# Kernel optimization log

Measured on AMD Instinct MI355X. Metric: run time of the kernel, lower is better.

## Reference

```python
import jax, jax.numpy as jnp
import numpy as np
from jax import lax

BN_EPS = 1e-5
PAD = ((2, 3), (1, 2))  # 'same' padding for kernel (6,4): H pad 5 -> (2,3), W pad 3 -> (1,2)
DN = ('NCHW', 'OIHW', 'NCHW')


def _conv_block(x, w, b, g, bt, m, v, pool):
    # pool(bn(relu(conv(pad(x))))) as in the torch module (eval-mode BN)
    x = lax.conv_general_dilated(x, w, (1, 1), PAD, dimension_numbers=DN)
    x = jax.nn.relu(x + b[None, :, None, None])
    scale = g / jnp.sqrt(v + BN_EPS)
    x = (x - m[None, :, None, None]) * scale[None, :, None, None] + bt[None, :, None, None]
    win = (1, 1) + pool
    return lax.reduce_window(x, -jnp.inf, lax.max, win, win, 'VALID')


def _fc_bn(x, w, b, g, bt, m, v):
    x = jax.nn.relu(x @ w.T + b)
    return (x - m) * (g / jnp.sqrt(v + BN_EPS)) + bt


def _apply_cnn(x, p):
    x = x[:, None, :, :]  # [N,1,72,64]
    x = _conv_block(x, p['conv1_w'], p['conv1_b'], p['bnc1_g'], p['bnc1_b'], p['bnc1_m'], p['bnc1_v'], (2, 2))
    x = _conv_block(x, p['conv2_w'], p['conv2_b'], p['bnc2_g'], p['bnc2_b'], p['bnc2_m'], p['bnc2_v'], (2, 2))
    x = _conv_block(x, p['conv3_w'], p['conv3_b'], p['bnc3_g'], p['bnc3_b'], p['bnc3_m'], p['bnc3_v'], (3, 4))
    x = x.reshape(x.shape[0], 6 * 4 * 64)  # NCHW contiguous flatten matches torch .view
    x = _fc_bn(x, p['fc1_w'], p['fc1_b'], p['bnf1_g'], p['bnf1_b'], p['bnf1_m'], p['bnf1_v'])
    x = _fc_bn(x, p['fc2_w'], p['fc2_b'], p['bnf2_g'], p['bnf2_b'], p['bnf2_m'], p['bnf2_v'])
    x = _fc_bn(x, p['fc3_w'], p['fc3_b'], p['bnf3_g'], p['bnf3_b'], p['bnf3_m'], p['bnf3_v'])
    # F.normalize(x, p=2, dim=1) with eps=1e-12
    nrm = jnp.linalg.norm(x, axis=1, keepdims=True)
    return x / jnp.maximum(nrm, 1e-12)


def _ssm(embeds):
    # pairwise L2 distances via Gram trick (replaces the O(n^2) python loop)
    sq = jnp.sum(embeds * embeds, axis=1)  # [n]
    d2 = sq[:, None] + sq[None, :] - 2.0 * (embeds @ embeds.T)
    dist = jnp.sqrt(jnp.maximum(d2, 1e-12))
    dist = jnp.where(d2 > 0, dist, 0.0)  # exact zeros on diagonal, nan-safe grad
    return dist / jnp.max(dist)


def setup_inputs() -> dict:
    key = jax.random.key(0)
    ks = iter(jax.random.split(key, 64))
    d = {'x': jax.random.normal(next(ks), (512, 72, 64), jnp.float32)}

    def nrm(shape, s=0.05):
        return jax.random.normal(next(ks), shape, jnp.float32) * s

    def add_bn(name, c):
        d[name + '_g'] = 1.0 + nrm((c,))
        d[name + '_b'] = nrm((c,))
        d[name + '_m'] = nrm((c,), 0.1)
        d[name + '_v'] = 0.5 + jax.random.uniform(next(ks), (c,), jnp.float32)

    d['conv1_w'] = nrm((16, 1, 6, 4), 0.2);  d['conv1_b'] = nrm((16,));  add_bn('bnc1', 16)
    d['conv2_w'] = nrm((32, 16, 6, 4), 0.1); d['conv2_b'] = nrm((32,));  add_bn('bnc2', 32)
    d['conv3_w'] = nrm((64, 32, 6, 4), 0.05); d['conv3_b'] = nrm((64,)); add_bn('bnc3', 64)
    d['fc1_w'] = nrm((512, 1536), 0.03); d['fc1_b'] = nrm((512,)); add_bn('bnf1', 512)
    d['fc2_w'] = nrm((256, 512), 0.05);  d['fc2_b'] = nrm((256,)); add_bn('bnf2', 256)
    d['fc3_w'] = nrm((128, 256), 0.07);  d['fc3_b'] = nrm((128,)); add_bn('bnf3', 128)
    return d


def reference(x,
              conv1_w, conv1_b, bnc1_g, bnc1_b, bnc1_m, bnc1_v,
              conv2_w, conv2_b, bnc2_g, bnc2_b, bnc2_m, bnc2_v,
              conv3_w, conv3_b, bnc3_g, bnc3_b, bnc3_m, bnc3_v,
              fc1_w, fc1_b, bnf1_g, bnf1_b, bnf1_m, bnf1_v,
              fc2_w, fc2_b, bnf2_g, bnf2_b, bnf2_m, bnf2_v,
              fc3_w, fc3_b, bnf3_g, bnf3_b, bnf3_m, bnf3_v):
    p = dict(conv1_w=conv1_w, conv1_b=conv1_b, bnc1_g=bnc1_g, bnc1_b=bnc1_b, bnc1_m=bnc1_m, bnc1_v=bnc1_v,
             conv2_w=conv2_w, conv2_b=conv2_b, bnc2_g=bnc2_g, bnc2_b=bnc2_b, bnc2_m=bnc2_m, bnc2_v=bnc2_v,
             conv3_w=conv3_w, conv3_b=conv3_b, bnc3_g=bnc3_g, bnc3_b=bnc3_b, bnc3_m=bnc3_m, bnc3_v=bnc3_v,
             fc1_w=fc1_w, fc1_b=fc1_b, bnf1_g=bnf1_g, bnf1_b=bnf1_b, bnf1_m=bnf1_m, bnf1_v=bnf1_v,
             fc2_w=fc2_w, fc2_b=fc2_b, bnf2_g=bnf2_g, bnf2_b=bnf2_b, bnf2_m=bnf2_m, bnf2_v=bnf2_v,
             fc3_w=fc3_w, fc3_b=fc3_b, bnf3_g=bnf3_g, bnf3_b=bnf3_b, bnf3_m=bnf3_m, bnf3_v=bnf3_v)
    embeds = _apply_cnn(x, p)  # [n, 128], L2-normalized
    return _ssm(embeds)        # [n, n]
```

## Files before the change

### kernel.cpp

```cpp
#include <hip/hip_runtime.h>
#include <hip/hip_bf16.h>
#include <math.h>


#define BN_EPS 1e-5f

typedef __attribute__((ext_vector_type(8))) short short8;
typedef __attribute__((ext_vector_type(4))) float f32x4;

__device__ __forceinline__ unsigned short f2bf(float f) {
    unsigned u = __float_as_uint(f);
    u += 0x7fffu + ((u >> 16) & 1u);
    return (unsigned short)(u >> 16);
}

__device__ __forceinline__ unsigned pkbf(float a, float b) {
    __hip_bfloat162 h = __float22bfloat162_rn(make_float2(a, b));
    return *reinterpret_cast<unsigned*>(&h);
}

__global__ __launch_bounds__(256) void repack_k(
    const float* __restrict__ w1, const float* __restrict__ w2,
    const float* __restrict__ w3,
    const float* __restrict__ fw1, const float* __restrict__ fw2,
    const float* __restrict__ fw3,
    unsigned short* __restrict__ wT1b,
    unsigned short* __restrict__ wT2b, unsigned short* __restrict__ wT3b,
    unsigned short* __restrict__ fw1b, unsigned short* __restrict__ fw2b,
    unsigned short* __restrict__ fw3b)
{
    int t = blockIdx.x * 256 + threadIdx.x;
    if (t < 512) {
        int k = t & 31, oc = t >> 5;
        wT1b[t] = (k < 24) ? f2bf(w1[oc * 24 + k]) : (unsigned short)0;
    }
    if (t < 12288) {
        int k = t & 31, oc = (t >> 5) & 31, kk = t >> 10;
        int ky = kk >> 1, kxp = kk & 1;
        int hi = k >> 4, ic = k & 15;
        int kx = 2 * kxp + hi;
        wT2b[t] = f2bf(w2[((oc * 16 + ic) * 6 + ky) * 4 + kx]);
    }
    if (t < 49152) {
        int ic = t & 31, oc = (t >> 5) & 63, kk = t >> 11;
        int ky = kk >> 2, kx = kk & 3;
        wT3b[t] = f2bf(w3[((oc * 32 + ic) * 6 + ky) * 4 + kx]);
    }
    if (t < 786432) fw1b[t] = f2bf(fw1[t]);
    if (t < 131072) fw2b[t] = f2bf(fw2[t]);
    if (t < 32768)  fw3b[t] = f2bf(fw3[t]);
}

__global__ __launch_bounds__(256) void conv1_mf(
    const float* __restrict__ x, const unsigned short* __restrict__ wT1,
    const float* __restrict__ bias, const float* __restrict__ g,
    const float* __restrict__ bt, const float* __restrict__ m,
    const float* __restrict__ v, unsigned short* __restrict__ out1,
    int nb0)
{
    __shared__ __align__(16) float pa[79 * 68];
    __shared__ __align__(16) float pb[79 * 68];
    const int tid = threadIdx.x, nl = blockIdx.x;
    {
        float2 z2 = make_float2(0.f, 0.f);
        float2* za = (float2*)pa; float2* zb = (float2*)pb;
        for (int i = tid; i < 2686; i += 256) { za[i] = z2; zb[i] = z2; }
    }
    unsigned short* ob = out1 + (size_t)nl * 23616;
    {
        uint4 z; z.x = z.y = z.z = z.w = 0u;
        for (int pc = tid; pc < 324; pc += 256) {
            int row, colc;
            if (pc < 180) { row = pc / 36; colc = pc % 36; if (row >= 2) row += 36; }
            else { int pz = pc - 180; row = 2 + (pz >> 2); colc = (pz & 3) ? 32 + (pz & 3) : 0; }
            uint4* d = (uint4*)(ob + ((size_t)row * 36 + colc) * 16);
            d[0] = z; d[1] = z;
        }
    }
    __syncthreads();
    {
        const float4* src = (const float4*)(x + (size_t)(nb0 + nl) * 4608);
        for (int i = tid; i < 1152; i += 256) {
            float4 val = src[i];
            int f = i * 4;
            int row = (f >> 6) + 2, c = (f & 63) + 1;
            float* a = pa + row * 68 + c;
            a[0] = val.x; a[1] = val.y; a[2] = val.z; a[3] = val.w;
            float2* b = (float2*)(pb + row * 68 + c + 1);
            b[0] = make_float2(val.x, val.y);
            b[1] = make_float2(val.z, val.w);
        }
    }
    const int lane = tid & 63, wave = tid >> 6;
    const int n = lane & 15, q = lane >> 4;
    float sc = g[n] * rsqrtf(v[n] + BN_EPS);
    float bb = bias[n];
    float mm = bt[n] - m[n] * sc;
    short8 bfr = *(const short8*)(wT1 + n * 32 + q * 8);
    __syncthreads();

    for (int i = 0; i < 72; ++i) {
        int t = wave * 72 + i;
        int pooled = 4 * t + (n >> 2);
        int ph = pooled >> 5, pw = pooled & 31;
        int py = (n >> 1) & 1, px = n & 1;
        int oh = 2 * ph + py, ow = 2 * pw + px;
        int r0 = (oh + 2 * q) * 68;
        const float* base = px ? (pb + r0 + ow + 1) : (pa + r0 + ow);
        float2 s00 = *(const float2*)(base);
        float2 s01 = *(const float2*)(base + 2);
        float2 s10 = *(const float2*)(base + 68);
        float2 s11 = *(const float2*)(base + 70);
        uint4 uu;
        uu.x = pkbf(s00.x, s00.y); uu.y = pkbf(s01.x, s01.y);
        uu.z = pkbf(s10.x, s10.y); uu.w = pkbf(s11.x, s11.y);
        short8 afr = *reinterpret_cast<short8*>(&uu);
        f32x4 acc = (f32x4){0.f, 0.f, 0.f, 0.f};
        acc = __builtin_amdgcn_mfma_f32_16x16x32_bf16(afr, bfr, acc, 0, 0, 0);
        int po = 4 * t + q;
        int oph = po >> 5, opw = po & 31;
        float mx = fmaxf(fmaxf(acc[0], acc[1]), fmaxf(acc[2], acc[3]));
        float val = fmaxf(mx + bb, 0.f) * sc + mm;
        ob[((size_t)(oph + 2) * 36 + (opw + 1)) * 16 + n] = f2bf(val);
    }
}

__global__ __launch_bounds__(256) void conv2_m(
    const unsigned short* __restrict__ in, const unsigned short* __restrict__ wT,
    const float* __restrict__ bias, const float* __restrict__ g,
    const float* __restrict__ bt, const float* __restrict__ m,
    const float* __restrict__ v, unsigned short* __restrict__ out)
{
    __shared__ __align__(16) unsigned short in_s[41 * 36 * 16];
    const int tid = threadIdx.x, nl = blockIdx.x;
    {
        const uint4* src = (const uint4*)(in + (size_t)nl * 23616);
        uint4* dst = (uint4*)in_s;
        for (int i = tid; i < 2952; i += 256) dst[i] = src[i];
    }
    unsigned short* ob = out + (size_t)nl * 15360;
    {
        uint4 z; z.x = z.y = z.z = z.w = 0u;
        for (int pc = tid; pc < 192; pc += 256) {
            int row, colc;
            if (pc < 120) { row = pc / 20; colc = pc % 20; if (row >= 2) row += 18; }
            else { int pz = pc - 120; row = 2 + (pz >> 2); colc = (pz & 3) ? 16 + (pz & 3) : 0; }
            uint4* d = (uint4*)(ob + ((size_t)row * 20 + colc) * 32);
            d[0] = z; d[1] = z; d[2] = z; d[3] = z;
        }
    }
    const int lane = tid & 63, wave = tid >> 6;
    const int n = lane & 15, q = lane >> 4;
    float bnb[2], bns[2], bnm[2];
#pragma unroll
    for (int nt = 0; nt < 2; ++nt) {
        int oc = nt * 16 + n;
        float sc = g[oc] * rsqrtf(v[oc] + BN_EPS);
        bnb[nt] = bias[oc]; bns[nt] = sc; bnm[nt] = bt[oc] - m[oc] * sc;
    }
    __syncthreads();

    for (int pass = 0; pass < 3; ++pass) {
        f32x4 acc[3][2][2];
#pragma unroll
        for (int j = 0; j < 3; ++j)
#pragma unroll
            for (int ab = 0; ab < 2; ++ab)
#pragma unroll
                for (int nt = 0; nt < 2; ++nt)
                    acc[j][ab][nt] = (f32x4){0.f, 0.f, 0.f, 0.f};

#pragma unroll
        for (int ky = 0; ky < 6; ++ky)
#pragma unroll
            for (int kxp = 0; kxp < 2; ++kxp) {
                int kk = ky * 2 + kxp;
                short8 bfr[2];
#pragma unroll
                for (int nt = 0; nt < 2; ++nt)
                    bfr[nt] = *(const short8*)(wT + (((size_t)kk * 32 + nt * 16 + n) * 32 + q * 8));
#pragma unroll
                for (int j = 0; j < 3; ++j) {
                    int pp = wave + 4 * (pass * 3 + j);
                    int ph = pp >> 1, half = pp & 1;
                    int col = half * 16 + n + 2 * kxp;
#pragma unroll
                    for (int ab = 0; ab < 2; ++ab) {
                        int row = 2 * ph + ab + ky;
                        short8 afr = *(const short8*)(in_s + (((size_t)row * 36 + col) * 16 + q * 8));
                        acc[j][ab][0] = __builtin_amdgcn_mfma_f32_16x16x32_bf16(afr, bfr[0], acc[j][ab][0], 0, 0, 0);
                        acc[j][ab][1] = __builtin_amdgcn_mfma_f32_16x16x32_bf16(afr, bfr[1], acc[j][ab][1], 0, 0, 0);
                    }
                }
            }
#pragma unroll
        for (int j = 0; j < 3; ++j) {
            int pp = wave + 4 * (pass * 3 + j);
            int ph = pp >> 1, half = pp & 1;
            int pw0 = half * 8 + q * 2;
#pragma unroll
            for (int nt = 0; nt < 2; ++nt) {
                int oc = nt * 16 + n;
                float p0 = fmaxf(fmaxf(acc[j][0][nt][0], acc[j][0][nt][1]),
                                 fmaxf(acc[j][1][nt][0], acc[j][1][nt][1]));
                float p1 = fmaxf(fmaxf(acc[j][0][nt][2], acc[j][0][nt][3]),
                                 fmaxf(acc[j][1][nt][2], acc[j][1][nt][3]));
                p0 = fmaxf(p0 + bnb[nt], 0.f) * bns[nt] + bnm[nt];
                p1 = fmaxf(p1 + bnb[nt], 0.f) * bns[nt] + bnm[nt];
                ob[((size_t)(ph + 2) * 20 + (pw0 + 1)) * 32 + oc] = f2bf(p0);
                ob[((size_t)(ph + 2) * 20 + (pw0 + 2)) * 32 + oc] = f2bf(p1);
            }
        }
    }
}

__global__ __launch_bounds__(384) void conv3_m(
    const unsigned short* __restrict__ in, const unsigned short* __restrict__ wT,
    const float* __restrict__ bias, const float* __restrict__ g,
    const float* __restrict__ bt, const float* __restrict__ m,
    const float* __restrict__ v, unsigned short* __restrict__ out3, int nb0)
{
    __shared__ __align__(16) unsigned short in_s[24 * 20 * 32];
    const int tid = threadIdx.x, nl = blockIdx.x;
    {
        const uint4* src = (const uint4*)(in + (size_t)nl * 15360);
        uint4* dst = (uint4*)in_s;
        for (int i = tid; i < 1920; i += 384) dst[i] = src[i];
    }
    const int lane = tid & 63, pr = tid >> 6;
    const int n = lane & 15, q = lane >> 4;
    float bnb[4], bns[4], bnm[4];
#pragma unroll
    for (int nt = 0; nt < 4; ++nt) {
        int oc = nt * 16 + n;
        float sc = g[oc] * rsqrtf(v[oc] + BN_EPS);
        bnb[nt] = bias[oc]; bns[nt] = sc; bnm[nt] = bt[oc] - m[oc] * sc;
    }
    __syncthreads();

    f32x4 acc[3][4];
#pragma unroll
    for (int r = 0; r < 3; ++r)
#pragma unroll
        for (int nt = 0; nt < 4; ++nt) acc[r][nt] = (f32x4){0.f, 0.f, 0.f, 0.f};

#pragma unroll
    for (int ky = 0; ky < 6; ++ky)
#pragma unroll
        for (int kx = 0; kx < 4; ++kx) {
            int kk = ky * 4 + kx;
            short8 bfr[4];
#pragma unroll
            for (int nt = 0; nt < 4; ++nt)
                bfr[nt] = *(const short8*)(wT + (((size_t)kk * 64 + nt * 16 + n) * 32 + q * 8));
#pragma unroll
            for (int r = 0; r < 3; ++r) {
                int row = 3 * pr + r + ky;
                int col = n + kx;
                short8 afr = *(const short8*)(in_s + (((size_t)row * 20 + col) * 32 + q * 8));
#pragma unroll
                for (int nt = 0; nt < 4; ++nt)
                    acc[r][nt] = __builtin_amdgcn_mfma_f32_16x16x32_bf16(afr, bfr[nt], acc[r][nt], 0, 0, 0);
            }
        }
    size_t ob = (size_t)(nb0 + nl) * 1536;
#pragma unroll
    for (int nt = 0; nt < 4; ++nt) {
        float mx = -3.4e38f;
#pragma unroll
        for (int r = 0; r < 3; ++r)
#pragma unroll
            for (int e = 0; e < 4; ++e) mx = fmaxf(mx, acc[r][nt][e]);
        float val = fmaxf(mx + bnb[nt], 0.f) * bns[nt] + bnm[nt];
        out3[ob + (size_t)(nt * 16 + n) * 24 + pr * 4 + q] = f2bf(val);
    }
}

__global__ __launch_bounds__(256) void fc_m(
    const unsigned short* __restrict__ A, const unsigned short* __restrict__ W,
    const float* __restrict__ bias, const float* __restrict__ g,
    const float* __restrict__ bt, const float* __restrict__ m,
    const float* __restrict__ v, unsigned short* __restrict__ out_b,
    float* __restrict__ out_f, int K, int N, int mode)
{
    const int tid = threadIdx.x;
    const int lane = tid & 63, wave = tid >> 6;
    const int n = lane & 15, q = lane >> 4;
    const int wr = wave >> 1, wc = wave & 1;
    const int r0 = blockIdx.y * 32 + wr * 16;
    const int c0 = blockIdx.x * 32 + wc * 16;
    const int col = c0 + n;

    float sc = g[col] * rsqrtf(v[col] + BN_EPS);
    float bb = bias[col];
    float mm = bt[col] - m[col] * sc;

    const unsigned short* Ap = A + (size_t)(r0 + n) * K + q * 8;
    const unsigned short* Bp = W + (size_t)col * K + q * 8;

    f32x4 acc = (f32x4){0.f, 0.f, 0.f, 0.f};
    for (int kk = 0; kk < K; kk += 64) {
        short8 a0 = *(const short8*)(Ap + kk);
        short8 b0 = *(const short8*)(Bp + kk);
        short8 a1 = *(const short8*)(Ap + kk + 32);
        short8 b1 = *(const short8*)(Bp + kk + 32);
        acc = __builtin_amdgcn_mfma_f32_16x16x32_bf16(a0, b0, acc, 0, 0, 0);
        acc = __builtin_amdgcn_mfma_f32_16x16x32_bf16(a1, b1, acc, 0, 0, 0);
    }
#pragma unroll
    for (int e = 0; e < 4; ++e) {
        int row = r0 + q * 4 + e;
        float val = fmaxf(acc[e] + bb, 0.f) * sc + mm;
        if (mode == 0) out_b[(size_t)row * N + col] = f2bf(val);
        else           out_f[(size_t)row * N + col] = val;
    }
}

__global__ __launch_bounds__(128) void norm_k(const float* __restrict__ f3,
                                              float* __restrict__ E,
                                              float* __restrict__ sq)
{
    __shared__ float red[2];
    const int row = blockIdx.x, tid = threadIdx.x;
    float vv = f3[row * 128 + tid];
    float s = vv * vv;
#pragma unroll
    for (int off = 32; off >= 1; off >>= 1) s += __shfl_down(s, off, 64);
    if ((tid & 63) == 0) red[tid >> 6] = s;
    __syncthreads();
    float total = red[0] + red[1];
    float nn = fmaxf(sqrtf(total), 1e-12f);
    E[row * 128 + tid] = vv / nn;
    if (tid == 0) sq[row] = total / (nn * nn);
}

__global__ __launch_bounds__(256) void dist_k(const float* __restrict__ E,
                                              const float* __restrict__ sq,
                                              float* __restrict__ D,
                                              unsigned* __restrict__ mxslot)
{
    __shared__ __align__(16) float Ei[16 * 132];
    __shared__ __align__(16) float Ej[16 * 132];
    __shared__ float red[256];
    const int tid = threadIdx.x;
    const int bi = blockIdx.y * 16, bj = blockIdx.x * 16;
    {
        int lr = tid >> 4, lc = (tid & 15) * 8;
        float4 a0 = *(const float4*)(E + (bi + lr) * 128 + lc);
        float4 a1 = *(const float4*)(E + (bi + lr) * 128 + lc + 4);
        *(float4*)(Ei + lr * 132 + lc) = a0;
        *(float4*)(Ei + lr * 132 + lc + 4) = a1;
        float4 b0 = *(const float4*)(E + (bj + lr) * 128 + lc);
        float4 b1 = *(const float4*)(E + (bj + lr) * 128 + lc + 4);
        *(float4*)(Ej + lr * 132 + lc) = b0;
        *(float4*)(Ej + lr * 132 + lc + 4) = b1;
    }
    __syncthreads();
    const int tx = tid & 15, ty = tid >> 4;
    float dot = 0.f;
#pragma unroll 4
    for (int k = 0; k < 128; k += 4) {
        float4 a = *(const float4*)(Ei + ty * 132 + k);
        float4 b = *(const float4*)(Ej + tx * 132 + k);
        dot = fmaf(a.x, b.x, dot); dot = fmaf(a.y, b.y, dot);
        dot = fmaf(a.z, b.z, dot); dot = fmaf(a.w, b.w, dot);
    }
    int i = bi + ty, j = bj + tx;
    float d2 = sq[i] + sq[j] - 2.f * dot;
    float dist = sqrtf(fmaxf(d2, 1e-12f));
    dist = (d2 > 0.f) ? dist : 0.f;
    if (i == j) dist = 0.f;
    D[i * 512 + j] = dist;
    red[tid] = dist;
    __syncthreads();
    for (int s2 = 128; s2 > 0; s2 >>= 1) {
        if (tid < s2) red[tid] = fmaxf(red[tid], red[tid + s2]);
        __syncthreads();
    }
    if (tid == 0) atomicMax(mxslot, __float_as_uint(red[0]));
}

__global__ __launch_bounds__(256) void scale_k(float* __restrict__ D,
                                               const unsigned* __restrict__ mxslot)
{
    int idx = blockIdx.x * 256 + threadIdx.x;
    float M = __uint_as_float(*mxslot);
    D[idx] = D[idx] / M;
}

extern "C" void kernel_launch(void* const* d_in, const int* in_sizes, int n_in,
                              void* d_out, int out_size, void* d_ws, size_t ws_size,
                              hipStream_t stream)
{
    (void)in_sizes; (void)n_in; (void)out_size;
    const float* x    = (const float*)d_in[0];
    const float* c1w  = (const float*)d_in[1];
    const float* c1b  = (const float*)d_in[2];
    const float* g1   = (const float*)d_in[3];
    const float* b1   = (const float*)d_in[4];
    const float* m1   = (const float*)d_in[5];
    const float* v1   = (const float*)d_in[6];
    const float* c2w  = (const float*)d_in[7];
    const float* c2b  = (const float*)d_in[8];
    const float* g2   = (const float*)d_in[9];
    const float* b2   = (const float*)d_in[10];
    const float* m2   = (const float*)d_in[11];
    const float* v2   = (const float*)d_in[12];
    const float* c3w  = (const float*)d_in[13];
    const float* c3b  = (const float*)d_in[14];
    const float* g3   = (const float*)d_in[15];
    const float* b3   = (const float*)d_in[16];
    const float* m3   = (const float*)d_in[17];
    const float* v3   = (const float*)d_in[18];
    const float* fw1  = (const float*)d_in[19];
    const float* fb1  = (const float*)d_in[20];
    const float* gf1  = (const float*)d_in[21];
    const float* bf1  = (const float*)d_in[22];
    const float* mf1  = (const float*)d_in[23];
    const float* vf1  = (const float*)d_in[24];
    const float* fw2  = (const float*)d_in[25];
    const float* fb2  = (const float*)d_in[26];
    const float* gf2  = (const float*)d_in[27];
    const float* bf2  = (const float*)d_in[28];
    const float* mf2  = (const float*)d_in[29];
    const float* vf2  = (const float*)d_in[30];
    const float* fw3  = (const float*)d_in[31];
    const float* fb3  = (const float*)d_in[32];
    const float* gf3  = (const float*)d_in[33];
    const float* bf3  = (const float*)d_in[34];
    const float* mf3  = (const float*)d_in[35];
    const float* vf3  = (const float*)d_in[36];

    float* ws = (float*)d_ws;
    float* f3v  = ws + 0;
    float* E    = ws + 65536;
    float* sq   = ws + 131072;
    unsigned* mx = (unsigned*)(ws + 131584);
    unsigned short* wT2b = (unsigned short*)(ws + 131600);
    unsigned short* wT3b = (unsigned short*)(ws + 137744);
    unsigned short* wT1b = (unsigned short*)(ws + 162320);
    unsigned short* fw1b = (unsigned short*)(ws + 162576);
    unsigned short* fw2b = (unsigned short*)(ws + 555792);
    unsigned short* fw3b = (unsigned short*)(ws + 621328);
    unsigned short* out3b= (unsigned short*)(ws + 637712);
    unsigned short* a1b  = (unsigned short*)(ws + 1030928);
    unsigned short* a2b  = (unsigned short*)(ws + 1162000);
    const size_t CH0 = 1227536;

    int Bc = 512;
    while (Bc > 4 && (size_t)CH0 * 4 + (size_t)Bc * 77952 > ws_size) Bc >>= 1;
    unsigned short* out1c = (unsigned short*)(ws + CH0);
    unsigned short* out2c = out1c + (size_t)Bc * 23616;

    float* out = (float*)d_out;

    hipMemsetAsync(mx, 0, 4, stream);
    repack_k<<<3072, 256, 0, stream>>>(c1w, c2w, c3w, fw1, fw2, fw3,
                                       wT1b, wT2b, wT3b, fw1b, fw2b, fw3b);
    for (int nb0 = 0; nb0 < 512; nb0 += Bc) {
        conv1_mf<<<Bc, 256, 0, stream>>>(x, wT1b, c1b, g1, b1, m1, v1, out1c, nb0);
        conv2_m<<<Bc, 256, 0, stream>>>(out1c, wT2b, c2b, g2, b2, m2, v2, out2c);
        conv3_m<<<Bc, 384, 0, stream>>>(out2c, wT3b, c3b, g3, b3, m3, v3, out3b, nb0);
    }
    fc_m<<<dim3(16, 16), 256, 0, stream>>>(out3b, fw1b, fb1, gf1, bf1, mf1, vf1,
                                           a1b, nullptr, 1536, 512, 0);
    fc_m<<<dim3(8, 16), 256, 0, stream>>>(a1b, fw2b, fb2, gf2, bf2, mf2, vf2,
                                          a2b, nullptr, 512, 256, 0);
    fc_m<<<dim3(4, 16), 256, 0, stream>>>(a2b, fw3b, fb3, gf3, bf3, mf3, vf3,
                                          nullptr, f3v, 256, 128, 1);
    norm_k<<<512, 128, 0, stream>>>(f3v, E, sq);
    dist_k<<<dim3(32, 32), 256, 0, stream>>>(E, sq, out, mx);
    scale_k<<<1024, 256, 0, stream>>>(out, mx);
}
```

Before: 239.5 us.

## Fuse three conv stages into one LDS-resident kernel and fuse FC chain with normalize

Merges conv1, conv2 and conv3 into a single 512-thread kernel per sample that keeps the intermediate activations in shared memory instead of global workspace. Conv1 input is converted to bf16 while staging, which halves LDS use and removes per-MFMA packing. The three FC layers and L2 normalization are fused into one kernel that keeps intermediates in LDS, and the memset is folded into repack. This removes global round-trips and several launches, at the cost of higher per-block LDS use and fewer blocks for the FC stage (32 blocks), which may lower parallelism.

```diff
diff --git a/kernel.cpp b/kernel.cpp
--- a/kernel.cpp
+++ b/kernel.cpp
@@ -1,5 +1,4 @@
 #include <hip/hip_runtime.h>
-#include <hip/hip_bf16.h>
 #include <math.h>
 
 
@@ -12,11 +11,6 @@
     unsigned u = __float_as_uint(f);
     u += 0x7fffu + ((u >> 16) & 1u);
     return (unsigned short)(u >> 16);
-}
-
-__device__ __forceinline__ unsigned pkbf(float a, float b) {
-    __hip_bfloat162 h = __float22bfloat162_rn(make_float2(a, b));
-    return *reinterpret_cast<unsigned*>(&h);
 }
 
 __global__ __launch_bounds__(256) void repack_k(
@@ -27,9 +21,10 @@
     unsigned short* __restrict__ wT1b,
     unsigned short* __restrict__ wT2b, unsigned short* __restrict__ wT3b,
     unsigned short* __restrict__ fw1b, unsigned short* __restrict__ fw2b,
-    unsigned short* __restrict__ fw3b)
+    unsigned short* __restrict__ fw3b, unsigned* __restrict__ mxslot)
 {
     int t = blockIdx.x * 256 + threadIdx.x;
+    if (t == 0) *mxslot = 0u;
     if (t < 512) {
         int k = t & 31, oc = t >> 5;
         wT1b[t] = (k < 24) ? f2bf(w1[oc * 24 + k]) : (unsigned short)0;
@@ -51,287 +46,276 @@
     if (t < 32768)  fw3b[t] = f2bf(fw3[t]);
 }
 
-__global__ __launch_bounds__(256) void conv1_mf(
+__global__ __launch_bounds__(512) void conv_all(
     const float* __restrict__ x, const unsigned short* __restrict__ wT1,
-    const float* __restrict__ bias, const float* __restrict__ g,
-    const float* __restrict__ bt, const float* __restrict__ m,
-    const float* __restrict__ v, unsigned short* __restrict__ out1,
-    int nb0)
-{
-    __shared__ __align__(16) float pa[79 * 68];
-    __shared__ __align__(16) float pb[79 * 68];
+    const unsigned short* __restrict__ wT2, const unsigned short* __restrict__ wT3,
+    const float* __restrict__ c1b, const float* __restrict__ g1,
+    const float* __restrict__ b1, const float* __restrict__ m1,
+    const float* __restrict__ v1,
+    const float* __restrict__ c2b, const float* __restrict__ g2,
+    const float* __restrict__ b2, const float* __restrict__ m2,
+    const float* __restrict__ v2,
+    const float* __restrict__ c3b, const float* __restrict__ g3,
+    const float* __restrict__ b3, const float* __restrict__ m3,
+    const float* __restrict__ v3,
+    unsigned short* __restrict__ out3)
+{
+    __shared__ __align__(16) unsigned short s_out1[41 * 36 * 16];
+    __shared__ __align__(16) unsigned short s_un[24 * 20 * 32];
     const int tid = threadIdx.x, nl = blockIdx.x;
+    const int lane = tid & 63, wave = tid >> 6;
+    const int n = lane & 15, q = lane >> 4;
+    unsigned short* pa = s_un;
+    unsigned short* pb = s_un + 5372;
+
     {
-        float2 z2 = make_float2(0.f, 0.f);
-        float2* za = (float2*)pa; float2* zb = (float2*)pb;
-        for (int i = tid; i < 2686; i += 256) { za[i] = z2; zb[i] = z2; }
-    }
-    unsigned short* ob = out1 + (size_t)nl * 23616;
-    {
-        uint4 z; z.x = z.y = z.z = z.w = 0u;
-        for (int pc = tid; pc < 324; pc += 256) {
+        unsigned* z32 = (unsigned*)s_un;
+        for (int i = tid; i < 5372; i += 512) z32[i] = 0u;
+        uint4 z4; z4.x = z4.y = z4.z = z4.w = 0u;
+        for (int pc = tid; pc < 324; pc += 512) {
             int row, colc;
             if (pc < 180) { row = pc / 36; colc = pc % 36; if (row >= 2) row += 36; }
             else { int pz = pc - 180; row = 2 + (pz >> 2); colc = (pz & 3) ? 32 + (pz & 3) : 0; }
-            uint4* d = (uint4*)(ob + ((size_t)row * 36 + colc) * 16);
-            d[0] = z; d[1] = z;
+            uint4* d = (uint4*)(s_out1 + ((size_t)row * 36 + colc) * 16);
+            d[0] = z4; d[1] = z4;
         }
     }
     __syncthreads();
     {
-        const float4* src = (const float4*)(x + (size_t)(nb0 + nl) * 4608);
-        for (int i = tid; i < 1152; i += 256) {
+        const float4* src = (const float4*)(x + (size_t)nl * 4608);
+        for (int i = tid; i < 1152; i += 512) {
             float4 val = src[i];
-            int f = i * 4;
-            int row = (f >> 6) + 2, c = (f & 63) + 1;
-            float* a = pa + row * 68 + c;
-            a[0] = val.x; a[1] = val.y; a[2] = val.z; a[3] = val.w;
-            float2* b = (float2*)(pb + row * 68 + c + 1);
-            b[0] = make_float2(val.x, val.y);
-            b[1] = make_float2(val.z, val.w);
-        }
-    }
-    const int lane = tid & 63, wave = tid >> 6;
-    const int n = lane & 15, q = lane >> 4;
-    float sc = g[n] * rsqrtf(v[n] + BN_EPS);
-    float bb = bias[n];
-    float mm = bt[n] - m[n] * sc;
-    short8 bfr = *(const short8*)(wT1 + n * 32 + q * 8);
-    __syncthreads();
-
-    for (int i = 0; i < 72; ++i) {
-        int t = wave * 72 + i;
+            int f = i * 4, row = (f >> 6) + 2, c = (f & 63) + 1;
+            unsigned short h0 = f2bf(val.x), h1 = f2bf(val.y);
+            unsigned short h2 = f2bf(val.z), h3 = f2bf(val.w);
+            unsigned short* ap = pa + row * 68 + c;
+            ap[0] = h0; ap[1] = h1; ap[2] = h2; ap[3] = h3;
+            unsigned* bp = (unsigned*)(pb + row * 68 + c + 1);
+            bp[0] = (unsigned)h0 | ((unsigned)h1 << 16);
+            bp[1] = (unsigned)h2 | ((unsigned)h3 << 16);
+        }
+    }
+    const float sc1 = g1[n] * rsqrtf(v1[n] + BN_EPS);
+    const float bb1 = c1b[n];
+    const float mm1 = b1[n] - m1[n] * sc1;
+    const short8 bfr1 = *(const short8*)(wT1 + n * 32 + q * 8);
+    __syncthreads();
+
+    for (int i = 0; i < 36; ++i) {
+        int t = wave * 36 + i;
         int pooled = 4 * t + (n >> 2);
         int ph = pooled >> 5, pw = pooled & 31;
         int py = (n >> 1) & 1, px = n & 1;
         int oh = 2 * ph + py, ow = 2 * pw + px;
         int r0 = (oh + 2 * q) * 68;
-        const float* base = px ? (pb + r0 + ow + 1) : (pa + r0 + ow);
-        float2 s00 = *(const float2*)(base);
-        float2 s01 = *(const float2*)(base + 2);
-        float2 s10 = *(const float2*)(base + 68);
-        float2 s11 = *(const float2*)(base + 70);
+        const unsigned* base = px ? (const unsigned*)(pb + r0 + ow + 1)
+                                  : (const unsigned*)(pa + r0 + ow);
         uint4 uu;
-        uu.x = pkbf(s00.x, s00.y); uu.y = pkbf(s01.x, s01.y);
-        uu.z = pkbf(s10.x, s10.y); uu.w = pkbf(s11.x, s11.y);
+        uu.x = base[0];  uu.y = base[1];
+        uu.z = base[34]; uu.w = base[35];
         short8 afr = *reinterpret_cast<short8*>(&uu);
         f32x4 acc = (f32x4){0.f, 0.f, 0.f, 0.f};
-        acc = __builtin_amdgcn_mfma_f32_16x16x32_bf16(afr, bfr, acc, 0, 0, 0);
-        int po = 4 * t + q;
-        int oph = po >> 5, opw = po & 31;
+        acc = __builtin_amdgcn_mfma_f32_16x16x32_bf16(afr, bfr1, acc, 0, 0, 0);
+        int po = 4 * t + q, oph = po >> 5, opw = po & 31;
         float mx = fmaxf(fmaxf(acc[0], acc[1]), fmaxf(acc[2], acc[3]));
-        float val = fmaxf(mx + bb, 0.f) * sc + mm;
-        ob[((size_t)(oph + 2) * 36 + (opw + 1)) * 16 + n] = f2bf(val);
-    }
-}
-
-__global__ __launch_bounds__(256) void conv2_m(
-    const unsigned short* __restrict__ in, const unsigned short* __restrict__ wT,
-    const float* __restrict__ bias, const float* __restrict__ g,
-    const float* __restrict__ bt, const float* __restrict__ m,
-    const float* __restrict__ v, unsigned short* __restrict__ out)
-{
-    __shared__ __align__(16) unsigned short in_s[41 * 36 * 16];
-    const int tid = threadIdx.x, nl = blockIdx.x;
+        float val = fmaxf(mx + bb1, 0.f) * sc1 + mm1;
+        s_out1[((oph + 2) * 36 + (opw + 1)) * 16 + n] = f2bf(val);
+    }
+    __syncthreads();
     {
-        const uint4* src = (const uint4*)(in + (size_t)nl * 23616);
-        uint4* dst = (uint4*)in_s;
-        for (int i = tid; i < 2952; i += 256) dst[i] = src[i];
-    }
-    unsigned short* ob = out + (size_t)nl * 15360;
-    {
-        uint4 z; z.x = z.y = z.z = z.w = 0u;
-        for (int pc = tid; pc < 192; pc += 256) {
+        uint4 z4; z4.x = z4.y = z4.z = z4.w = 0u;
+        for (int pc = tid; pc < 192; pc += 512) {
             int row, colc;
             if (pc < 120) { row = pc / 20; colc = pc % 20; if (row >= 2) row += 18; }
             else { int pz = pc - 120; row = 2 + (pz >> 2); colc = (pz & 3) ? 16 + (pz & 3) : 0; }
-            uint4* d = (uint4*)(ob + ((size_t)row * 20 + colc) * 32);
-            d[0] = z; d[1] = z; d[2] = z; d[3] = z;
-        }
-    }
-    const int lane = tid & 63, wave = tid >> 6;
-    const int n = lane & 15, q = lane >> 4;
-    float bnb[2], bns[2], bnm[2];
+            uint4* d = (uint4*)(s_un + ((size_t)row * 20 + colc) * 32);
+            d[0] = z4; d[1] = z4; d[2] = z4; d[3] = z4;
+        }
+    }
+    float bnb2[2], bns2[2], bnm2[2];
 #pragma unroll
     for (int nt = 0; nt < 2; ++nt) {
         int oc = nt * 16 + n;
-        float sc = g[oc] * rsqrtf(v[oc] + BN_EPS);
-        bnb[nt] = bias[oc]; bns[nt] = sc; bnm[nt] = bt[oc] - m[oc] * sc;
-    }
-    __syncthreads();
-
-    for (int pass = 0; pass < 3; ++pass) {
-        f32x4 acc[3][2][2];
-#pragma unroll
-        for (int j = 0; j < 3; ++j)
-#pragma unroll
-            for (int ab = 0; ab < 2; ++ab)
-#pragma unroll
-                for (int nt = 0; nt < 2; ++nt)
-                    acc[j][ab][nt] = (f32x4){0.f, 0.f, 0.f, 0.f};
-
+        float sc = g2[oc] * rsqrtf(v2[oc] + BN_EPS);
+        bnb2[nt] = c2b[oc]; bns2[nt] = sc; bnm2[nt] = b2[oc] - m2[oc] * sc;
+    }
+    __syncthreads();
+
+    for (int pp = wave; pp < 36; pp += 8) {
+        int ph = pp >> 1, half = pp & 1;
+        f32x4 acc[2][2];
+#pragma unroll
+        for (int ab = 0; ab < 2; ++ab)
+#pragma unroll
+            for (int nt = 0; nt < 2; ++nt) acc[ab][nt] = (f32x4){0.f, 0.f, 0.f, 0.f};
 #pragma unroll
         for (int ky = 0; ky < 6; ++ky)
 #pragma unroll
             for (int kxp = 0; kxp < 2; ++kxp) {
                 int kk = ky * 2 + kxp;
-                short8 bfr[2];
-#pragma unroll
-                for (int nt = 0; nt < 2; ++nt)
-                    bfr[nt] = *(const short8*)(wT + (((size_t)kk * 32 + nt * 16 + n) * 32 + q * 8));
-#pragma unroll
-                for (int j = 0; j < 3; ++j) {
-                    int pp = wave + 4 * (pass * 3 + j);
-                    int ph = pp >> 1, half = pp & 1;
-                    int col = half * 16 + n + 2 * kxp;
-#pragma unroll
-                    for (int ab = 0; ab < 2; ++ab) {
-                        int row = 2 * ph + ab + ky;
-                        short8 afr = *(const short8*)(in_s + (((size_t)row * 36 + col) * 16 + q * 8));
-                        acc[j][ab][0] = __builtin_amdgcn_mfma_f32_16x16x32_bf16(afr, bfr[0], acc[j][ab][0], 0, 0, 0);
-                        acc[j][ab][1] = __builtin_amdgcn_mfma_f32_16x16x32_bf16(afr, bfr[1], acc[j][ab][1], 0, 0, 0);
-                    }
+                short8 w0 = *(const short8*)(wT2 + ((size_t)(kk * 32 + n) * 32) + q * 8);
+                short8 w1 = *(const short8*)(wT2 + ((size_t)(kk * 32 + 16 + n) * 32) + q * 8);
+                int col = half * 16 + n + 2 * kxp;
+#pragma unroll
+                for (int ab = 0; ab < 2; ++ab) {
+                    int row = 2 * ph + ab + ky;
+                    short8 afr = *(const short8*)(s_out1 + ((size_t)(row * 36 + col) * 16) + q * 8);
+                    acc[ab][0] = __builtin_amdgcn_mfma_f32_16x16x32_bf16(afr, w0, acc[ab][0], 0, 0, 0);
+                    acc[ab][1] = __builtin_amdgcn_mfma_f32_16x16x32_bf16(afr, w1, acc[ab][1], 0, 0, 0);
                 }
             }
-#pragma unroll
-        for (int j = 0; j < 3; ++j) {
-            int pp = wave + 4 * (pass * 3 + j);
-            int ph = pp >> 1, half = pp & 1;
-            int pw0 = half * 8 + q * 2;
-#pragma unroll
-            for (int nt = 0; nt < 2; ++nt) {
-                int oc = nt * 16 + n;
-                float p0 = fmaxf(fmaxf(acc[j][0][nt][0], acc[j][0][nt][1]),
-                                 fmaxf(acc[j][1][nt][0], acc[j][1][nt][1]));
-                float p1 = fmaxf(fmaxf(acc[j][0][nt][2], acc[j][0][nt][3]),
-                                 fmaxf(acc[j][1][nt][2], acc[j][1][nt][3]));
-                p0 = fmaxf(p0 + bnb[nt], 0.f) * bns[nt] + bnm[nt];
-                p1 = fmaxf(p1 + bnb[nt], 0.f) * bns[nt] + bnm[nt];
-                ob[((size_t)(ph + 2) * 20 + (pw0 + 1)) * 32 + oc] = f2bf(p0);
-                ob[((size_t)(ph + 2) * 20 + (pw0 + 2)) * 32 + oc] = f2bf(p1);
+        int pw0 = half * 8 + q * 2;
+#pragma unroll
+        for (int nt = 0; nt < 2; ++nt) {
+            int oc = nt * 16 + n;
+            float p0 = fmaxf(fmaxf(acc[0][nt][0], acc[0][nt][1]),
+                             fmaxf(acc[1][nt][0], acc[1][nt][1]));
+            float p1 = fmaxf(fmaxf(acc[0][nt][2], acc[0][nt][3]),
+                             fmaxf(acc[1][nt][2], acc[1][nt][3]));
+            p0 = fmaxf(p0 + bnb2[nt], 0.f) * bns2[nt] + bnm2[nt];
+            p1 = fmaxf(p1 + bnb2[nt], 0.f) * bns2[nt] + bnm2[nt];
+            s_un[((size_t)(ph + 2) * 20 + (pw0 + 1)) * 32 + oc] = f2bf(p0);
+            s_un[((size_t)(ph + 2) * 20 + (pw0 + 2)) * 32 + oc] = f2bf(p1);
+        }
+    }
+    __syncthreads();
+
+    for (int ch = wave; ch < 12; ch += 8) {
+        int pr = ch >> 1, nth = ch & 1;
+        f32x4 acc[3][2];
+#pragma unroll
+        for (int r = 0; r < 3; ++r)
+#pragma unroll
+            for (int t2 = 0; t2 < 2; ++t2) acc[r][t2] = (f32x4){0.f, 0.f, 0.f, 0.f};
+#pragma unroll
+        for (int ky = 0; ky < 6; ++ky)
+#pragma unroll
+            for (int kx = 0; kx < 4; ++kx) {
+                int kk = ky * 4 + kx;
+                short8 w0 = *(const short8*)(wT3 + ((size_t)(kk * 64 + nth * 32 + n) * 32) + q * 8);
+                short8 w1 = *(const short8*)(wT3 + ((size_t)(kk * 64 + nth * 32 + 16 + n) * 32) + q * 8);
+#pragma unroll
+                for (int r = 0; r < 3; ++r) {
+                    int row = 3 * pr + r + ky;
+                    int col = n + kx;
+                    short8 afr = *(const short8*)(s_un + ((size_t)(row * 20 + col) * 32) + q * 8);
+                    acc[r][0] = __builtin_amdgcn_mfma_f32_16x16x32_bf16(afr, w0, acc[r][0], 0, 0, 0);
+                    acc[r][1] = __builtin_amdgcn_mfma_f32_16x16x32_bf16(afr, w1, acc[r][1], 0, 0, 0);
+                }
             }
-        }
-    }
-}
-
-__global__ __launch_bounds__(384) void conv3_m(
-    const unsigned short* __restrict__ in, const unsigned short* __restrict__ wT,
-    const float* __restrict__ bias, const float* __restrict__ g,
-    const float* __restrict__ bt, const float* __restrict__ m,
-    const float* __restrict__ v, unsigned short* __restrict__ out3, int nb0)
-{
-    __shared__ __align__(16) unsigned short in_s[24 * 20 * 32];
-    const int tid = threadIdx.x, nl = blockIdx.x;
-    {
-        const uint4* src = (const uint4*)(in + (size_t)nl * 15360);
-        uint4* dst = (uint4*)in_s;
-        for (int i = tid; i < 1920; i += 384) dst[i] = src[i];
-    }
-    const int lane = tid & 63, pr = tid >> 6;
-    const int n = lane & 15, q = lane >> 4;
-    float bnb[4], bns[4], bnm[4];
-#pragma unroll
-    for (int nt = 0; nt < 4; ++nt) {
-        int oc = nt * 16 + n;
-        float sc = g[oc] * rsqrtf(v[oc] + BN_EPS);
-        bnb[nt] = bias[oc]; bns[nt] = sc; bnm[nt] = bt[oc] - m[oc] * sc;
-    }
-    __syncthreads();
-
-    f32x4 acc[3][4];
-#pragma unroll
-    for (int r = 0; r < 3; ++r)
-#pragma unroll
-        for (int nt = 0; nt < 4; ++nt) acc[r][nt] = (f32x4){0.f, 0.f, 0.f, 0.f};
-
-#pragma unroll
-    for (int ky = 0; ky < 6; ++ky)
-#pragma unroll
-        for (int kx = 0; kx < 4; ++kx) {
-            int kk = ky * 4 + kx;
-            short8 bfr[4];
-#pragma unroll
-            for (int nt = 0; nt < 4; ++nt)
-                bfr[nt] = *(const short8*)(wT + (((size_t)kk * 64 + nt * 16 + n) * 32 + q * 8));
-#pragma unroll
-            for (int r = 0; r < 3; ++r) {
-                int row = 3 * pr + r + ky;
-                int col = n + kx;
-                short8 afr = *(const short8*)(in_s + (((size_t)row * 20 + col) * 32 + q * 8));
-#pragma unroll
-                for (int nt = 0; nt < 4; ++nt)
-                    acc[r][nt] = __builtin_amdgcn_mfma_f32_16x16x32_bf16(afr, bfr[nt], acc[r][nt], 0, 0, 0);
-            }
-        }
-    size_t ob = (size_t)(nb0 + nl) * 1536;
-#pragma unroll
-    for (int nt = 0; nt < 4; ++nt) {
-        float mx = -3.4e38f;
-#pragma unroll
-        for (int r = 0; r < 3; ++r)
-#pragma unroll
-            for (int e = 0; e < 4; ++e) mx = fmaxf(mx, acc[r][nt][e]);
-        float val = fmaxf(mx + bnb[nt], 0.f) * bns[nt] + bnm[nt];
-        out3[ob + (size_t)(nt * 16 + n) * 24 + pr * 4 + q] = f2bf(val);
-    }
-}
-
-__global__ __launch_bounds__(256) void fc_m(
-    const unsigned short* __restrict__ A, const unsigned short* __restrict__ W,
-    const float* __restrict__ bias, const float* __restrict__ g,
-    const float* __restrict__ bt, const float* __restrict__ m,
-    const float* __restrict__ v, unsigned short* __restrict__ out_b,
-    float* __restrict__ out_f, int K, int N, int mode)
-{
+        size_t ob = (size_t)nl * 1536;
+#pragma unroll
+        for (int t2 = 0; t2 < 2; ++t2) {
+            int oc = nth * 32 + t2 * 16 + n;
+            float sc = g3[oc] * rsqrtf(v3[oc] + BN_EPS);
+            float mx = -3.4e38f;
+#pragma unroll
+            for (int r = 0; r < 3; ++r)
+#pragma unroll
+                for (int e = 0; e < 4; ++e) mx = fmaxf(mx, acc[r][t2][e]);
+            float val = fmaxf(mx + c3b[oc], 0.f) * sc + (b3[oc] - m3[oc] * sc);
+            out3[ob + (size_t)oc * 24 + pr * 4 + q] = f2bf(val);
+        }
+    }
+}
+
+__global__ __launch_bounds__(256) void fcn_k(
+    const unsigned short* __restrict__ A,
+    const unsigned short* __restrict__ W1, const float* __restrict__ fb1,
+    const float* __restrict__ gf1, const float* __restrict__ bf1,
+    const float* __restrict__ mf1, const float* __restrict__ vf1,
+    const unsigned short* __restrict__ W2, const float* __restrict__ fb2,
+    const float* __restrict__ gf2, const float* __restrict__ bf2,
+    const float* __restrict__ mf2, const float* __restrict__ vf2,
+    const unsigned short* __restrict__ W3, const float* __restrict__ fb3,
+    const float* __restrict__ gf3, const float* __restrict__ bf3,
+    const float* __restrict__ mf3, const float* __restrict__ vf3,
+    float* __restrict__ E, float* __restrict__ sq)
+{
+    __shared__ __align__(16) unsigned short z1[16 * 512];
+    __shared__ __align__(16) unsigned short z2[16 * 256];
+    __shared__ __align__(16) float z3[16 * 128];
     const int tid = threadIdx.x;
     const int lane = tid & 63, wave = tid >> 6;
     const int n = lane & 15, q = lane >> 4;
-    const int wr = wave >> 1, wc = wave & 1;
-    const int r0 = blockIdx.y * 32 + wr * 16;
-    const int c0 = blockIdx.x * 32 + wc * 16;
-    const int col = c0 + n;
-
-    float sc = g[col] * rsqrtf(v[col] + BN_EPS);
-    float bb = bias[col];
-    float mm = bt[col] - m[col] * sc;
-
-    const unsigned short* Ap = A + (size_t)(r0 + n) * K + q * 8;
-    const unsigned short* Bp = W + (size_t)col * K + q * 8;
-
-    f32x4 acc = (f32x4){0.f, 0.f, 0.f, 0.f};
-    for (int kk = 0; kk < K; kk += 64) {
-        short8 a0 = *(const short8*)(Ap + kk);
-        short8 b0 = *(const short8*)(Bp + kk);
-        short8 a1 = *(const short8*)(Ap + kk + 32);
-        short8 b1 = *(const short8*)(Bp + kk + 32);
-        acc = __builtin_amdgcn_mfma_f32_16x16x32_bf16(a0, b0, acc, 0, 0, 0);
-        acc = __builtin_amdgcn_mfma_f32_16x16x32_bf16(a1, b1, acc, 0, 0, 0);
-    }
-#pragma unroll
-    for (int e = 0; e < 4; ++e) {
-        int row = r0 + q * 4 + e;
-        float val = fmaxf(acc[e] + bb, 0.f) * sc + mm;
-        if (mode == 0) out_b[(size_t)row * N + col] = f2bf(val);
-        else           out_f[(size_t)row * N + col] = val;
-    }
-}
-
-__global__ __launch_bounds__(128) void norm_k(const float* __restrict__ f3,
-                                              float* __restrict__ E,
-                                              float* __restrict__ sq)
-{
-    __shared__ float red[2];
-    const int row = blockIdx.x, tid = threadIdx.x;
-    float vv = f3[row * 128 + tid];
-    float s = vv * vv;
-#pragma unroll
-    for (int off = 32; off >= 1; off >>= 1) s += __shfl_down(s, off, 64);
-    if ((tid & 63) == 0) red[tid >> 6] = s;
-    __syncthreads();
-    float total = red[0] + red[1];
-    float nn = fmaxf(sqrtf(total), 1e-12f);
-    E[row * 128 + tid] = vv / nn;
-    if (tid == 0) sq[row] = total / (nn * nn);
+    const int r0 = blockIdx.x * 16;
+
+    for (int nt = wave; nt < 32; nt += 4) {
+        int col = nt * 16 + n;
+        float sc = gf1[col] * rsqrtf(vf1[col] + BN_EPS);
+        float bb = fb1[col], mm = bf1[col] - mf1[col] * sc;
+        const unsigned short* Ap = A + (size_t)(r0 + n) * 1536 + q * 8;
+        const unsigned short* Bp = W1 + (size_t)col * 1536 + q * 8;
+        f32x4 acc = (f32x4){0.f, 0.f, 0.f, 0.f};
+        for (int kk = 0; kk < 1536; kk += 64) {
+            short8 a0 = *(const short8*)(Ap + kk);
+            short8 b0 = *(const short8*)(Bp + kk);
+            short8 a1 = *(const short8*)(Ap + kk + 32);
+            short8 b1 = *(const short8*)(Bp + kk + 32);
+            acc = __builtin_amdgcn_mfma_f32_16x16x32_bf16(a0, b0, acc, 0, 0, 0);
+            acc = __builtin_amdgcn_mfma_f32_16x16x32_bf16(a1, b1, acc, 0, 0, 0);
+        }
+#pragma unroll
+        for (int e = 0; e < 4; ++e) {
+            float val = fmaxf(acc[e] + bb, 0.f) * sc + mm;
+            z1[(q * 4 + e) * 512 + col] = f2bf(val);
+        }
+    }
+    __syncthreads();
+    for (int nt = wave; nt < 16; nt += 4) {
+        int col = nt * 16 + n;
+        float sc = gf2[col] * rsqrtf(vf2[col] + BN_EPS);
+        float bb = fb2[col], mm = bf2[col] - mf2[col] * sc;
+        const unsigned short* Bp = W2 + (size_t)col * 512 + q * 8;
+        f32x4 acc = (f32x4){0.f, 0.f, 0.f, 0.f};
+        for (int kk = 0; kk < 512; kk += 32) {
+            short8 a0 = *(const short8*)(z1 + n * 512 + kk + q * 8);
+            short8 b0 = *(const short8*)(Bp + kk);
+            acc = __builtin_amdgcn_mfma_f32_16x16x32_bf16(a0, b0, acc, 0, 0, 0);
+        }
+#pragma unroll
+        for (int e = 0; e < 4; ++e) {
+            float val = fmaxf(acc[e] + bb, 0.f) * sc + mm;
+            z2[(q * 4 + e) * 256 + col] = f2bf(val);
+        }
+    }
+    __syncthreads();
+    for (int nt = wave; nt < 8; nt += 4) {
+        int col = nt * 16 + n;
+        float sc = gf3[col] * rsqrtf(vf3[col] + BN_EPS);
+        float bb = fb3[col], mm = bf3[col] - mf3[col] * sc;
+        const unsigned short* Bp = W3 + (size_t)col * 256 + q * 8;
+        f32x4 acc = (f32x4){0.f, 0.f, 0.f, 0.f};
+        for (int kk = 0; kk < 256; kk += 32) {
+            short8 a0 = *(const short8*)(z2 + n * 256 + kk + q * 8);
+            short8 b0 = *(const short8*)(Bp + kk);
+            acc = __builtin_amdgcn_mfma_f32_16x16x32_bf16(a0, b0, acc, 0, 0, 0);
+        }
+#pragma unroll
+        for (int e = 0; e < 4; ++e) {
+            float val = fmaxf(acc[e] + bb, 0.f) * sc + mm;
+            z3[(q * 4 + e) * 128 + col] = val;
+        }
+    }
+    __syncthreads();
+    {
+        int row_l = tid >> 4, j = tid & 15;
+        float4 v0 = *(const float4*)(z3 + row_l * 128 + j * 8);
+        float4 v1 = *(const float4*)(z3 + row_l * 128 + j * 8 + 4);
+        float s = v0.x * v0.x + v0.y * v0.y + v0.z * v0.z + v0.w * v0.w
+                + v1.x * v1.x + v1.y * v1.y + v1.z * v1.z + v1.w * v1.w;
+#pragma unroll
+        for (int off = 1; off < 16; off <<= 1) s += __shfl_xor(s, off, 16);
+        float nn = fmaxf(sqrtf(s), 1e-12f);
+        float inv = 1.f / nn;
+        int row = r0 + row_l;
+        float4 e0, e1;
+        e0.x = v0.x * inv; e0.y = v0.y * inv; e0.z = v0.z * inv; e0.w = v0.w * inv;
+        e1.x = v1.x * inv; e1.y = v1.y * inv; e1.z = v1.z * inv; e1.w = v1.w * inv;
+        *(float4*)(E + (size_t)row * 128 + j * 8) = e0;
+        *(float4*)(E + (size_t)row * 128 + j * 8 + 4) = e1;
+        if (j == 0) sq[row] = s * inv * inv;
+    }
 }
 
 __global__ __launch_bounds__(256) void dist_k(const float* __restrict__ E,
@@ -392,7 +376,7 @@
                               void* d_out, int out_size, void* d_ws, size_t ws_size,
                               hipStream_t stream)
 {
-    (void)in_sizes; (void)n_in; (void)out_size;
+    (void)in_sizes; (void)n_in; (void)out_size; (void)ws_size;
     const float* x    = (const float*)d_in[0];
     const float* c1w  = (const float*)d_in[1];
     const float* c1b  = (const float*)d_in[2];
@@ -432,43 +416,30 @@
     const float* vf3  = (const float*)d_in[36];
 
     float* ws = (float*)d_ws;
-    float* f3v  = ws + 0;
-    float* E    = ws + 65536;
-    float* sq   = ws + 131072;
-    unsigned* mx = (unsigned*)(ws + 131584);
-    unsigned short* wT2b = (unsigned short*)(ws + 131600);
-    unsigned short* wT3b = (unsigned short*)(ws + 137744);
-    unsigned short* wT1b = (unsigned short*)(ws + 162320);
-    unsigned short* fw1b = (unsigned short*)(ws + 162576);
-    unsigned short* fw2b = (unsigned short*)(ws + 555792);
-    unsigned short* fw3b = (unsigned short*)(ws + 621328);
-    unsigned short* out3b= (unsigned short*)(ws + 637712);
-    unsigned short* a1b  = (unsigned short*)(ws + 1030928);
-    unsigned short* a2b  = (unsigned short*)(ws + 1162000);
-    const size_t CH0 = 1227536;
-
-    int Bc = 512;
-    while (Bc > 4 && (size_t)CH0 * 4 + (size_t)Bc * 77952 > ws_size) Bc >>= 1;
-    unsigned short* out1c = (unsigned short*)(ws + CH0);
-    unsigned short* out2c = out1c + (size_t)Bc * 23616;
+    float* E    = ws + 0;
+    float* sq   = ws + 65536;
+    unsigned* mx = (unsigned*)(ws + 66048);
+    unsigned short* wT1b = (unsigned short*)(ws + 66064);
+    unsigned short* wT2b = (unsigned short*)(ws + 66320);
+    unsigned short* wT3b = (unsigned short*)(ws + 72464);
+    unsigned short* fw1b = (unsigned short*)(ws + 97040);
+    unsigned short* fw2b = (unsigned short*)(ws + 490256);
+    unsigned short* fw3b = (unsigned short*)(ws + 555792);
+    unsigned short* out3b= (unsigned short*)(ws + 572176);
 
     float* out = (float*)d_out;
 
-    hipMemsetAsync(mx, 0, 4, stream);
     repack_k<<<3072, 256, 0, stream>>>(c1w, c2w, c3w, fw1, fw2, fw3,
-                                       wT1b, wT2b, wT3b, fw1b, fw2b, fw3b);
-    for (int nb0 = 0; nb0 < 512; nb0 += Bc) {
-        conv1_mf<<<Bc, 256, 0, stream>>>(x, wT1b, c1b, g1, b1, m1, v1, out1c, nb0);
-        conv2_m<<<Bc, 256, 0, stream>>>(out1c, wT2b, c2b, g2, b2, m2, v2, out2c);
-        conv3_m<<<Bc, 384, 0, stream>>>(out2c, wT3b, c3b, g3, b3, m3, v3, out3b, nb0);
-    }
-    fc_m<<<dim3(16, 16), 256, 0, stream>>>(out3b, fw1b, fb1, gf1, bf1, mf1, vf1,
-                                           a1b, nullptr, 1536, 512, 0);
-    fc_m<<<dim3(8, 16), 256, 0, stream>>>(a1b, fw2b, fb2, gf2, bf2, mf2, vf2,
-                                          a2b, nullptr, 512, 256, 0);
-    fc_m<<<dim3(4, 16), 256, 0, stream>>>(a2b, fw3b, fb3, gf3, bf3, mf3, vf3,
-                                          nullptr, f3v, 256, 128, 1);
-    norm_k<<<512, 128, 0, stream>>>(f3v, E, sq);
+                                       wT1b, wT2b, wT3b, fw1b, fw2b, fw3b, mx);
+    conv_all<<<512, 512, 0, stream>>>(x, wT1b, wT2b, wT3b,
+                                      c1b, g1, b1, m1, v1,
+                                      c2b, g2, b2, m2, v2,
+                                      c3b, g3, b3, m3, v3, out3b);
+    fcn_k<<<32, 256, 0, stream>>>(out3b,
+                                  fw1b, fb1, gf1, bf1, mf1, vf1,
+                                  fw2b, fb2, gf2, bf2, mf2, vf2,
+                                  fw3b, fb3, gf3, bf3, mf3, vf3,
+                                  E, sq);
     dist_k<<<dim3(32, 32), 256, 0, stream>>>(E, sq, out, mx);
     scale_k<<<1024, 256, 0, stream>>>(out, mx);
 }
```

After: 277.5 us. 15.9% more time.
